# Performance work log

Measured on AMD Instinct MI355X. Metric: run time of the kernel, lower is better.

## Reference

```python
import jax, jax.numpy as jnp
import numpy as np

L_CHUNK = 5   # frames per camera chunk (hardcoded L=5 in similarity())
N_CAMS = 6    # len(cam_list)
TOP_K = 8     # hardcoded K=8 in similarity()
HEADS = 8


def setup_inputs() -> dict:
    key = jax.random.key(0)
    ks = jax.random.split(key, 5)
    B, M, N, C = 1, L_CHUNK * N_CAMS, 261, 2048  # M = S*P = 30 multiview token groups
    scale = 0.02
    tokens = jax.random.normal(ks[0], (B, M, N, C), dtype=jnp.float32)
    Wq = jax.random.normal(ks[1], (C, C), dtype=jnp.float32) * scale
    Wk = jax.random.normal(ks[2], (C, C), dtype=jnp.float32) * scale
    Wv = jax.random.normal(ks[3], (C, C), dtype=jnp.float32) * scale
    Wo = jax.random.normal(ks[4], (C, C), dtype=jnp.float32) * scale
    return {"tokens": tokens, "Wq": Wq, "Wk": Wk, "Wv": Wv, "Wo": Wo}


def _similarity(pose_tokens):
    # pose_tokens: [B, M, C] -> block-diag-biased softmax sim + topk neighbors
    sim = jnp.einsum('bmc,bnc->bmn', pose_tokens, pose_tokens)
    block = jnp.kron(jnp.eye(N_CAMS, dtype=sim.dtype),
                     jnp.ones((L_CHUNK, L_CHUNK), dtype=sim.dtype))  # [M, M]
    sim = sim + 10000.0 * block
    probs = jax.nn.softmax(sim, axis=-1)
    vals, idx = jax.lax.top_k(probs, TOP_K)  # [B, M, K]
    return vals, idx


def reference(tokens, Wq, Wk, Wv, Wo):
    B, M, N, C = tokens.shape
    H = HEADS
    d = C // H
    # similarity + topk over camera/pose tokens (token index 0 of each group)
    vals, idx = _similarity(tokens[:, :, 0, :])
    # gather K neighbor token groups per (batch, group): [B, M, K, N, C]
    nbr = jax.vmap(lambda t, i: t[i])(tokens, idx)
    nbr = nbr.reshape(B, M, TOP_K * N, C)
    q = (tokens @ Wq).reshape(B, M, N, H, d)
    k = (nbr @ Wk).reshape(B, M, TOP_K * N, H, d)
    v = (nbr @ Wv).reshape(B, M, TOP_K * N, H, d)
    scores = jnp.einsum('bmqhd,bmkhd->bmhqk', q, k) / jnp.sqrt(jnp.asarray(d, q.dtype))
    # weight each neighbor's tokens by its topk similarity value (log-bias)
    bias = jnp.repeat(jnp.log(vals + 1e-6), N, axis=-1)  # [B, M, K*N]
    scores = scores + bias[:, :, None, None, :]
    attn = jax.nn.softmax(scores, axis=-1)
    out = jnp.einsum('bmhqk,bmkhd->bmqhd', attn, v).reshape(B, M, N, C)
    return tokens + out @ Wo
```

## Files before the change

### kernel.cpp

```cpp
#include <hip/hip_runtime.h>
#include <stdint.h>

#define MTOK 7830
#define MPAD 7936
#define CD   2048
#define VTC  7920
#define AS1 __attribute__((address_space(1)))
#define AS3 __attribute__((address_space(3)))

typedef unsigned short u16;
typedef __bf16 bf16x8 __attribute__((ext_vector_type(8)));
typedef float f32x4 __attribute__((ext_vector_type(4)));
typedef unsigned short u16x8 __attribute__((ext_vector_type(8)));

__device__ __forceinline__ u16 f2bf(float f) {
  unsigned x = __float_as_uint(f);
  return (u16)((x + 0x7fffu + ((x >> 16) & 1u)) >> 16);
}

__device__ __forceinline__ void gld16(const u16* g, u16* l) {
  __builtin_amdgcn_global_load_lds((AS1 const unsigned int*)(g), (AS3 unsigned int*)(l), 16, 0, 0);
}

__global__ void cvt_tokens(const float* __restrict__ T, u16* __restrict__ O) {
  int row = blockIdx.x;
  size_t base = (size_t)row * CD + threadIdx.x * 8;
  u16x8 o = {0,0,0,0,0,0,0,0};
  if (row < MTOK) {
    const float* s = T + base;
    #pragma unroll
    for (int j = 0; j < 8; ++j) o[j] = f2bf(s[j]);
  }
  *(u16x8*)&O[base] = o;
}

__global__ void cvt_w(const float* __restrict__ Wq, const float* __restrict__ Wk,
                      const float* __restrict__ Wv, const float* __restrict__ Wo,
                      u16* __restrict__ WqkvT, u16* __restrict__ WoT) {
  __shared__ float tile[32][33];
  int k0 = blockIdx.x * 32;
  int n0 = blockIdx.y * 32;
  const float* W; u16* Dst; int nl0, dr0;
  if (n0 < 2048)      { W = Wq; Dst = WqkvT; nl0 = n0;        dr0 = n0; }
  else if (n0 < 4096) { W = Wk; Dst = WqkvT; nl0 = n0 - 2048; dr0 = n0; }
  else if (n0 < 6144) { W = Wv; Dst = WqkvT; nl0 = n0 - 4096; dr0 = n0; }
  else                { W = Wo; Dst = WoT;   nl0 = n0 - 6144; dr0 = n0 - 6144; }
  int tx = threadIdx.x, ty = threadIdx.y;
  #pragma unroll
  for (int i = 0; i < 4; ++i)
    tile[ty + i*8][tx] = W[(size_t)(k0 + ty + i*8) * CD + nl0 + tx];
  __syncthreads();
  #pragma unroll
  for (int i = 0; i < 4; ++i) {
    int n = ty + i*8;
    Dst[(size_t)(dr0 + n) * CD + k0 + tx] = f2bf(tile[tx][n]);
  }
}

__global__ void posesim(const float* __restrict__ tok, float* __restrict__ sim) {
  int mm = blockIdx.y, nn = blockIdx.x;
  const float* a = tok + (size_t)mm * 261 * CD;
  const float* b = tok + (size_t)nn * 261 * CD;
  int tid = threadIdx.x;
  float p = 0.f;
  for (int j = tid; j < CD; j += 256) p += a[j] * b[j];
  __shared__ float red[256];
  red[tid] = p; __syncthreads();
  for (int s = 128; s > 0; s >>= 1) { if (tid < s) red[tid] += red[tid + s]; __syncthreads(); }
  if (tid == 0) sim[mm*30 + nn] = red[0] + (((mm/5) == (nn/5)) ? 10000.0f : 0.0f);
}

__global__ void topk_bias(const float* __restrict__ sim, float* __restrict__ bias,
                          int* __restrict__ idxo) {
  int m = threadIdx.x;
  if (m >= 30) return;
  float p[30];
  float mx = -1e30f;
  for (int j = 0; j < 30; ++j) { p[j] = sim[m*30 + j]; mx = fmaxf(mx, p[j]); }
  float z = 0.f;
  for (int j = 0; j < 30; ++j) { p[j] = __expf(p[j] - mx); z += p[j]; }
  float inv = 1.0f / z;
  for (int j = 0; j < 30; ++j) p[j] *= inv;
  for (int k = 0; k < 8; ++k) {
    int bj = 0; float bv = p[0];
    for (int j = 1; j < 30; ++j) if (p[j] > bv) { bv = p[j]; bj = j; }
    idxo[m*8 + k] = bj;
    bias[m*8 + k] = logf(bv + 1e-6f);
    p[bj] = -1.0f;
  }
}

template<int EPI>
__global__ __launch_bounds__(512) void gemm_bt(
    const u16* __restrict__ A, const u16* __restrict__ Bt,
    u16* __restrict__ Cq, u16* __restrict__ Cv,
    const float* __restrict__ resid, float* __restrict__ Dout, int K)
{
  __shared__ u16 Al[2][256 * 64];
  __shared__ u16 Bl[2][256 * 64];
  int tid = threadIdx.x, lane = tid & 63, wid = tid >> 6;
  int lo4 = lane & 15, hi2 = lane >> 4;
  int bn = blockIdx.x, bm = blockIdx.y;
  int wy = wid >> 2, wx = wid & 3;
  int r8 = lane >> 3, c8 = lane & 7;

  f32x4 acc[8][4] = {};

  size_t aofs[4], bofs[4];
  #pragma unroll
  for (int j = 0; j < 4; ++j) {
    int row = wid*32 + j*8 + r8;
    int sw = 8 * (c8 ^ (row & 7));
    aofs[j] = (size_t)(bm*256 + row) * K + sw;
    bofs[j] = (size_t)(bn*256 + row) * K + sw;
  }
  int ldst = wid * 2048;

  int nK = K >> 6;
  #pragma unroll
  for (int j = 0; j < 4; ++j) {
    gld16(A  + aofs[j], &Al[0][ldst + j*512]);
    gld16(Bt + bofs[j], &Bl[0][ldst + j*512]);
  }

  for (int t = 0; t < nK; ++t) {
    __syncthreads();
    const u16* Ac = Al[t & 1];
    const u16* Bc = Bl[t & 1];
    u16* An = Al[(t + 1) & 1];
    u16* Bn = Bl[(t + 1) & 1];
    bool pf = (t + 1) < nK;
    size_t kn = (size_t)(t + 1) << 6;

    bf16x8 bvk[4];
    #pragma unroll
    for (int p = 0; p < 4; ++p) {
      int kk = p >> 1, mg = p & 1;
      if (p == 0 && pf) {
        gld16(A  + kn + aofs[0], &An[ldst]);
        gld16(A  + kn + aofs[1], &An[ldst + 512]);
        gld16(Bt + kn + bofs[0], &Bn[ldst]);
        gld16(Bt + kn + bofs[1], &Bn[ldst + 512]);
      }
      if (p == 1 && pf) {
        gld16(A  + kn + aofs[2], &An[ldst + 1024]);
        gld16(A  + kn + aofs[3], &An[ldst + 1536]);
        gld16(Bt + kn + bofs[2], &Bn[ldst + 1024]);
        gld16(Bt + kn + bofs[3], &Bn[ldst + 1536]);
      }
      if (mg == 0) {
        #pragma unroll
        for (int ni = 0; ni < 4; ++ni) {
          int br = wx*64 + ni*16 + lo4;
          bvk[ni] = *(const bf16x8*)&Bc[br*64 + 8*((kk*4 + hi2) ^ (br & 7))];
        }
      }
      bf16x8 av[4];
      #pragma unroll
      for (int mi = 0; mi < 4; ++mi) {
        int ar = wy*128 + mg*64 + mi*16 + lo4;
        av[mi] = *(const bf16x8*)&Ac[ar*64 + 8*((kk*4 + hi2) ^ (ar & 7))];
      }
      __builtin_amdgcn_s_setprio(1);
      #pragma unroll
      for (int mi = 0; mi < 4; ++mi)
        #pragma unroll
        for (int ni = 0; ni < 4; ++ni)
          acc[mg*4 + mi][ni] =
              __builtin_amdgcn_mfma_f32_16x16x32_bf16(av[mi], bvk[ni], acc[mg*4 + mi][ni], 0, 0, 0);
      __builtin_amdgcn_s_setprio(0);
    }
  }

  int gm0 = bm*256 + wy*128;
  int gn0 = bn*256 + wx*64;
  #pragma unroll
  for (int mi = 0; mi < 8; ++mi) {
    #pragma unroll
    for (int ni = 0; ni < 4; ++ni) {
      int gmb = gm0 + mi*16 + hi2*4;
      int gn  = gn0 + ni*16 + lo4;
      #pragma unroll
      for (int r = 0; r < 4; ++r) {
        float v = acc[mi][ni][r];
        int gm = gmb + r;
        if (EPI == 0) {
          if (gn < 4096) {
            Cq[(size_t)gm * 4096 + gn] = f2bf(v);
          } else if (gm < MTOK) {
            int g = gm / 261, tk = gm - g * 261;
            Cv[(size_t)(gn - 4096) * VTC + g * 264 + tk] = f2bf(v);
          }
        } else {
          if (gm < MTOK) {
            size_t off = (size_t)gm * CD + gn;
            Dout[off] = resid[off] + v;
          }
        }
      }
    }
  }
}

__global__ __launch_bounds__(1024) void attn_main(
    const u16* __restrict__ QK,
    const u16* __restrict__ VtG,
    const float* __restrict__ bias, const int* __restrict__ idx,
    u16* __restrict__ AO)
{
  int h = blockIdx.x, m = blockIdx.y;
  int tid = threadIdx.x, lane = tid & 63, wid = tid >> 6;
  int lo4 = lane & 15, hi2 = lane >> 4;

  __shared__ u16 Kl[2][32 * 256];
  __shared__ u16 Vl[2][256 * 32];
  __shared__ u16 Pl[16][16 * 50];
  __shared__ float bias_s[8];
  __shared__ int   idx_s[8];
  if (tid < 8) {
    bias_s[tid] = bias[m*8 + tid] * 1.4426950408889634f;
    idx_s[tid]  = idx[m*8 + tid];
  }

  int qrow = m*261 + wid*16 + lo4;
  bf16x8 qf[8];
  #pragma unroll
  for (int kk = 0; kk < 8; ++kk)
    qf[kk] = *(const bf16x8*)&QK[(size_t)qrow * 4096 + h*256 + kk*32 + hi2*8];

  int rt = 2*wid + (lane >> 5);
  size_t kof = (size_t)rt * 4096 + 2048 + h*256 + 8*((lane & 31) ^ (rt & 7));
  int vdr = 16*wid + (lane >> 2);
  size_t vof = (size_t)(h*256 + vdr) * VTC + 8*((lane & 3) ^ ((vdr >> 1) & 3));

  f32x4 O[16] = {};
  float srun[4] = {0.f, 0.f, 0.f, 0.f};
  const float SC = 0.09016844f;

  {
    int ig0 = idx[m*8];
    gld16(QK + (size_t)(ig0*261) * 4096 + kof, &Kl[0][wid*512]);
    gld16(VtG + (size_t)(ig0*264) + vof,       &Vl[0][wid*512]);
  }

  int vswz = 8 * (hi2 ^ ((lo4 >> 1) & 3));
  int kxb  = (lo4 >> 2) & 1;
  int kswz = 8 * (hi2 ^ (lo4 & 3));

  for (int it = 0; it < 72; ++it) {
    __syncthreads();
    if (it + 1 < 72) {
      int tn = it + 1;
      int gg = tn / 9;
      int tok0n = (tn - gg*9) * 32;
      int ign = idx_s[gg];
      gld16(QK + (size_t)(ign*261 + tok0n) * 4096 + kof, &Kl[tn & 1][wid*512]);
      gld16(VtG + (size_t)(ign*264 + tok0n) + vof,       &Vl[tn & 1][wid*512]);
    }
    {
      int gg = it / 9;
      int tok0 = (it - gg*9) * 32;
      float bgl = bias_s[gg];
      const u16* Kb = Kl[it & 1];
      const u16* Vb = Vl[it & 1];

      f32x4 s0v = {0,0,0,0}, s1v = {0,0,0,0};
      __builtin_amdgcn_s_setprio(1);
      #pragma unroll
      for (int kk = 0; kk < 8; ++kk) {
        int off = lo4*256 + 32*(kk ^ kxb) + kswz;
        bf16x8 kb0 = *(const bf16x8*)&Kb[off];
        bf16x8 kb1 = *(const bf16x8*)&Kb[off + 16*256];
        s0v = __builtin_amdgcn_mfma_f32_16x16x32_bf16(qf[kk], kb0, s0v, 0, 0, 0);
        s1v = __builtin_amdgcn_mfma_f32_16x16x32_bf16(qf[kk], kb1, s1v, 0, 0, 0);
      }
      __builtin_amdgcn_s_setprio(0);
      bool v0 = (tok0 + lo4) < 261, v1 = (tok0 + 16 + lo4) < 261;
      float p0[4], p1[4];
      #pragma unroll
      for (int r = 0; r < 4; ++r) {
        float e0 = __builtin_exp2f(fmaf(s0v[r], SC, bgl));
        float e1 = __builtin_exp2f(fmaf(s1v[r], SC, bgl));
        e0 = v0 ? e0 : 0.f;
        e1 = v1 ? e1 : 0.f;
        srun[r] += e0 + e1;
        p0[r] = e0; p1[r] = e1;
      }
      u16* Pw = Pl[wid];
      #pragma unroll
      for (int r = 0; r < 4; ++r) {
        Pw[(hi2*4 + r)*50 + lo4]      = f2bf(p0[r]);
        Pw[(hi2*4 + r)*50 + 16 + lo4] = f2bf(p1[r]);
      }
      bf16x8 pa = *(const bf16x8*)&Pw[lo4*50 + hi2*8];
      __builtin_amdgcn_s_setprio(1);
      #pragma unroll
      for (int o = 0; o < 16; ++o) {
        bf16x8 vv = *(const bf16x8*)&Vb[(o*16 + lo4)*32 + vswz];
        O[o] = __builtin_amdgcn_mfma_f32_16x16x32_bf16(pa, vv, O[o], 0, 0, 0);
      }
      __builtin_amdgcn_s_setprio(0);
    }
  }

  #pragma unroll
  for (int r = 0; r < 4; ++r) {
    float s = srun[r];
    s += __shfl_xor(s, 1);
    s += __shfl_xor(s, 2);
    s += __shfl_xor(s, 4);
    s += __shfl_xor(s, 8);
    srun[r] = 1.0f / s;
  }
  #pragma unroll
  for (int o = 0; o < 16; ++o) {
    #pragma unroll
    for (int r = 0; r < 4; ++r) {
      int qq = wid*16 + hi2*4 + r;
      AO[(size_t)(m*261 + qq) * CD + h*256 + o*16 + lo4] = f2bf(O[o][r] * srun[r]);
    }
  }
}

__global__ __launch_bounds__(256) void attn_tail(
    const u16* __restrict__ QK, const u16* __restrict__ VtG,
    const float* __restrict__ bias, const int* __restrict__ idx,
    u16* __restrict__ AO)
{
  int h = blockIdx.x, m = blockIdx.y;
  int tid = threadIdx.x, lane = tid & 63, wid = tid >> 6;
  int lo4 = lane & 15, hi2 = lane >> 4;

  __shared__ float Om[4][16][256];
  __shared__ float Sm[4][16];
  __shared__ u16 Pl[4][16 * 50];

  int q = 256 + lo4;
  bool qv = q < 261;
  int qrow = m*261 + (qv ? q : 0);
  bf16x8 qf[8];
  #pragma unroll
  for (int kk = 0; kk < 8; ++kk) {
    u16x8 u = {0,0,0,0,0,0,0,0};
    if (qv) u = *(const u16x8*)&QK[(size_t)qrow * 4096 + h*256 + kk*32 + hi2*8];
    qf[kk] = __builtin_bit_cast(bf16x8, u);
  }

  f32x4 O[16] = {};
  float srun[4] = {0.f, 0.f, 0.f, 0.f};
  const float SC = 0.09016844f;

  for (int it = wid; it < 72; it += 4) {
    int gg = it / 9;
    int tok0 = (it - gg*9) * 32;
    int ig = idx[m*8 + gg];
    float bgl = bias[m*8 + gg] * 1.4426950408889634f;
    const u16* kbase = QK + (size_t)(ig*261 + tok0) * 4096 + 2048 + h*256;
    f32x4 s0v = {0,0,0,0}, s1v = {0,0,0,0};
    #pragma unroll
    for (int kk = 0; kk < 8; ++kk) {
      bf16x8 kb0 = *(const bf16x8*)&kbase[(size_t)lo4 * 4096 + kk*32 + hi2*8];
      bf16x8 kb1 = *(const bf16x8*)&kbase[(size_t)(16 + lo4) * 4096 + kk*32 + hi2*8];
      s0v = __builtin_amdgcn_mfma_f32_16x16x32_bf16(qf[kk], kb0, s0v, 0, 0, 0);
      s1v = __builtin_amdgcn_mfma_f32_16x16x32_bf16(qf[kk], kb1, s1v, 0, 0, 0);
    }
    bool v0 = (tok0 + lo4) < 261, v1 = (tok0 + 16 + lo4) < 261;
    float p0[4], p1[4];
    #pragma unroll
    for (int r = 0; r < 4; ++r) {
      float e0 = __builtin_exp2f(fmaf(s0v[r], SC, bgl));
      float e1 = __builtin_exp2f(fmaf(s1v[r], SC, bgl));
      e0 = v0 ? e0 : 0.f;
      e1 = v1 ? e1 : 0.f;
      srun[r] += e0 + e1;
      p0[r] = e0; p1[r] = e1;
    }
    u16* Pw = Pl[wid];
    #pragma unroll
    for (int r = 0; r < 4; ++r) {
      Pw[(hi2*4 + r)*50 + lo4]      = f2bf(p0[r]);
      Pw[(hi2*4 + r)*50 + 16 + lo4] = f2bf(p1[r]);
    }
    bf16x8 pa = *(const bf16x8*)&Pw[lo4*50 + hi2*8];
    const u16* vbase = VtG + (size_t)(h*256) * VTC + ig*264 + tok0;
    #pragma unroll
    for (int o = 0; o < 16; ++o) {
      bf16x8 vv = *(const bf16x8*)&vbase[(size_t)(o*16 + lo4) * VTC + hi2*8];
      O[o] = __builtin_amdgcn_mfma_f32_16x16x32_bf16(pa, vv, O[o], 0, 0, 0);
    }
  }

  #pragma unroll
  for (int r = 0; r < 4; ++r) {
    float s = srun[r];
    s += __shfl_xor(s, 1);
    s += __shfl_xor(s, 2);
    s += __shfl_xor(s, 4);
    s += __shfl_xor(s, 8);
    srun[r] = s;
  }
  #pragma unroll
  for (int o = 0; o < 16; ++o)
    #pragma unroll
    for (int r = 0; r < 4; ++r)
      Om[wid][hi2*4 + r][o*16 + lo4] = O[o][r];
  if (lo4 == 0) {
    #pragma unroll
    for (int r = 0; r < 4; ++r) Sm[wid][hi2*4 + r] = srun[r];
  }
  __syncthreads();
  if (wid == 0) {
    #pragma unroll
    for (int o = 0; o < 16; ++o) {
      #pragma unroll
      for (int r = 0; r < 4; ++r) {
        int row = hi2*4 + r;
        int qq = 256 + row;
        if (qq < 261) {
          int c = o*16 + lo4;
          float v = Om[0][row][c] + Om[1][row][c] + Om[2][row][c] + Om[3][row][c];
          float s = Sm[0][row] + Sm[1][row] + Sm[2][row] + Sm[3][row];
          AO[(size_t)(m*261 + qq) * CD + h*256 + c] = f2bf(v / s);
        }
      }
    }
  }
}

extern "C" void kernel_launch(void* const* d_in, const int* in_sizes, int n_in,
                              void* d_out, int out_size, void* d_ws, size_t ws_size,
                              hipStream_t stream) {
  const float* tokens = (const float*)d_in[0];
  const float* Wq = (const float*)d_in[1];
  const float* Wk = (const float*)d_in[2];
  const float* Wv = (const float*)d_in[3];
  const float* Wo = (const float*)d_in[4];
  float* out = (float*)d_out;
  char* ws = (char*)d_ws;

  constexpr size_t OFF_TOKBF = 0;
  constexpr size_t OFF_WQKVT = OFF_TOKBF + (size_t)MPAD * CD * 2;
  constexpr size_t OFF_WOT   = OFF_WQKVT + (size_t)6144 * CD * 2;
  constexpr size_t OFF_QK    = OFF_WOT   + (size_t)CD * CD * 2;
  constexpr size_t OFF_VTG   = OFF_QK    + (size_t)MPAD * 4096 * 2;
  constexpr size_t OFF_AO    = OFF_VTG   + (size_t)CD * VTC * 2 + 4096;
  constexpr size_t OFF_SIM   = OFF_AO    + (size_t)MPAD * CD * 2;
  constexpr size_t OFF_BIAS  = OFF_SIM   + 4096;
  constexpr size_t OFF_IDX   = OFF_BIAS  + 1024;

  u16* tokBf  = (u16*)(ws + OFF_TOKBF);
  u16* WqkvT  = (u16*)(ws + OFF_WQKVT);
  u16* WoT    = (u16*)(ws + OFF_WOT);
  u16* QKbuf  = (u16*)(ws + OFF_QK);
  u16* VtG    = (u16*)(ws + OFF_VTG);
  u16* attnO  = (u16*)(ws + OFF_AO);
  float* simw = (float*)(ws + OFF_SIM);
  float* bw   = (float*)(ws + OFF_BIAS);
  int*   iw   = (int*)(ws + OFF_IDX);

  cvt_tokens<<<MPAD, 256, 0, stream>>>(tokens, tokBf);
  cvt_w<<<dim3(64, 256), dim3(32, 8), 0, stream>>>(Wq, Wk, Wv, Wo, WqkvT, WoT);
  posesim<<<dim3(30, 30), 256, 0, stream>>>(tokens, simw);
  topk_bias<<<1, 32, 0, stream>>>(simw, bw, iw);
  gemm_bt<0><<<dim3(24, 31), 512, 0, stream>>>(tokBf, WqkvT, QKbuf, VtG, nullptr, nullptr, CD);
  attn_tail<<<dim3(8, 30), 256, 0, stream>>>(QKbuf, VtG, bw, iw, attnO);
  attn_main<<<dim3(8, 30), 1024, 0, stream>>>(QKbuf, VtG, bw, iw, attnO);
  gemm_bt<1><<<dim3(8, 31), 512, 0, stream>>>(attnO, WoT, nullptr, nullptr, tokens, out, CD);
}
```

Before: 742.0 us.

## Deepen GEMM prefetch to two tiles ahead and remap blocks for L2 locality

The bf16 GEMM main loop now keeps two K-tiles in flight: both LDS buffers are filled up front and the refill for tile t+2 is issued after the current buffer is consumed. A partial vmcnt wait plus an explicit s_barrier replaces the full __syncthreads, so global loads overlap more of the MFMA work. Block indices are also remapped with a stride-8 interleave, meant to spread or group tiles across XCDs for better cache reuse. This relies on hand-placed waitcnt and barriers being correct. The remap assumes the grid size is divisible by 8.

```diff
diff --git a/kernel.cpp b/kernel.cpp
--- a/kernel.cpp
+++ b/kernel.cpp
@@ -100,7 +100,10 @@
   __shared__ u16 Bl[2][256 * 64];
   int tid = threadIdx.x, lane = tid & 63, wid = tid >> 6;
   int lo4 = lane & 15, hi2 = lane >> 4;
-  int bn = blockIdx.x, bm = blockIdx.y;
+  int lin = blockIdx.y * gridDim.x + blockIdx.x;
+  int q8  = (gridDim.x * gridDim.y) >> 3;
+  int lin2 = (lin & 7) * q8 + (lin >> 3);
+  int bn = lin2 % gridDim.x, bm = lin2 / gridDim.x;
   int wy = wid >> 2, wx = wid & 3;
   int r8 = lane >> 3, c8 = lane & 7;
 
@@ -122,53 +125,67 @@
     gld16(A  + aofs[j], &Al[0][ldst + j*512]);
     gld16(Bt + bofs[j], &Bl[0][ldst + j*512]);
   }
+  #pragma unroll
+  for (int j = 0; j < 4; ++j) {
+    gld16(A  + 64 + aofs[j], &Al[1][ldst + j*512]);
+    gld16(Bt + 64 + bofs[j], &Bl[1][ldst + j*512]);
+  }
 
   for (int t = 0; t < nK; ++t) {
-    __syncthreads();
+    if (t + 1 < nK) asm volatile("s_waitcnt vmcnt(8)" ::: "memory");
+    else            asm volatile("s_waitcnt vmcnt(0)" ::: "memory");
+    __builtin_amdgcn_sched_barrier(0);
+    __builtin_amdgcn_s_barrier();
+    __builtin_amdgcn_sched_barrier(0);
+
     const u16* Ac = Al[t & 1];
     const u16* Bc = Bl[t & 1];
-    u16* An = Al[(t + 1) & 1];
-    u16* Bn = Bl[(t + 1) & 1];
-    bool pf = (t + 1) < nK;
-    size_t kn = (size_t)(t + 1) << 6;
-
-    bf16x8 bvk[4];
-    #pragma unroll
-    for (int p = 0; p < 4; ++p) {
-      int kk = p >> 1, mg = p & 1;
-      if (p == 0 && pf) {
-        gld16(A  + kn + aofs[0], &An[ldst]);
-        gld16(A  + kn + aofs[1], &An[ldst + 512]);
-        gld16(Bt + kn + bofs[0], &Bn[ldst]);
-        gld16(Bt + kn + bofs[1], &Bn[ldst + 512]);
-      }
-      if (p == 1 && pf) {
-        gld16(A  + kn + aofs[2], &An[ldst + 1024]);
-        gld16(A  + kn + aofs[3], &An[ldst + 1536]);
-        gld16(Bt + kn + bofs[2], &Bn[ldst + 1024]);
-        gld16(Bt + kn + bofs[3], &Bn[ldst + 1536]);
-      }
-      if (mg == 0) {
-        #pragma unroll
-        for (int ni = 0; ni < 4; ++ni) {
-          int br = wx*64 + ni*16 + lo4;
-          bvk[ni] = *(const bf16x8*)&Bc[br*64 + 8*((kk*4 + hi2) ^ (br & 7))];
-        }
-      }
-      bf16x8 av[4];
+
+    bf16x8 bv[4][2];
+    #pragma unroll
+    for (int ni = 0; ni < 4; ++ni) {
+      int br = wx*64 + ni*16 + lo4;
+      #pragma unroll
+      for (int kk = 0; kk < 2; ++kk)
+        bv[ni][kk] = *(const bf16x8*)&Bc[br*64 + 8*((kk*4 + hi2) ^ (br & 7))];
+    }
+
+    #pragma unroll
+    for (int mg = 0; mg < 2; ++mg) {
+      bf16x8 av[4][2];
       #pragma unroll
       for (int mi = 0; mi < 4; ++mi) {
         int ar = wy*128 + mg*64 + mi*16 + lo4;
-        av[mi] = *(const bf16x8*)&Ac[ar*64 + 8*((kk*4 + hi2) ^ (ar & 7))];
+        #pragma unroll
+        for (int kk = 0; kk < 2; ++kk)
+          av[mi][kk] = *(const bf16x8*)&Ac[ar*64 + 8*((kk*4 + hi2) ^ (ar & 7))];
       }
       __builtin_amdgcn_s_setprio(1);
       #pragma unroll
-      for (int mi = 0; mi < 4; ++mi)
+      for (int kk = 0; kk < 2; ++kk)
         #pragma unroll
-        for (int ni = 0; ni < 4; ++ni)
-          acc[mg*4 + mi][ni] =
-              __builtin_amdgcn_mfma_f32_16x16x32_bf16(av[mi], bvk[ni], acc[mg*4 + mi][ni], 0, 0, 0);
+        for (int mi = 0; mi < 4; ++mi)
+          #pragma unroll
+          for (int ni = 0; ni < 4; ++ni)
+            acc[mg*4 + mi][ni] = __builtin_amdgcn_mfma_f32_16x16x32_bf16(
+                av[mi][kk], bv[ni][kk], acc[mg*4 + mi][ni], 0, 0, 0);
       __builtin_amdgcn_s_setprio(0);
+      if (mg == 0) {
+        __builtin_amdgcn_s_barrier();
+      } else {
+        __builtin_amdgcn_sched_barrier(0);
+        if (t + 2 < nK) {
+          size_t kn = (size_t)(t + 2) << 6;
+          u16* An = Al[t & 1];
+          u16* Bn = Bl[t & 1];
+          #pragma unroll
+          for (int j = 0; j < 4; ++j) {
+            gld16(A  + kn + aofs[j], &An[ldst + j*512]);
+            gld16(Bt + kn + bofs[j], &Bn[ldst + j*512]);
+          }
+        }
+        __builtin_amdgcn_sched_barrier(0);
+      }
     }
   }
 
```

Measured after the change: 682.8 us. -8.0%, faster.
